# Kernel optimization log

Hardware: AMD Instinct MI355X
Metric: run time of the kernel (lower is better)

## Reference

```python
import jax, jax.numpy as jnp
import numpy as np

B, S, D, H, F = 2, 2048, 1024, 16, 4096
DK = D // H
EPS = 1e-6


def _ln(x, g, b):
    mu = jnp.mean(x, axis=-1, keepdims=True)
    var = jnp.mean(jnp.square(x - mu), axis=-1, keepdims=True)
    return (x - mu) * jax.lax.rsqrt(var + EPS) * g + b


def setup_inputs() -> dict:
    key = jax.random.key(0)
    ks = jax.random.split(key, 8)
    sc = 0.02
    return {
        "x": jax.random.normal(ks[0], (B, S, D), jnp.float32),
        "wq": jax.random.normal(ks[1], (D, D), jnp.float32) * sc,
        "bq": jnp.zeros((D,), jnp.float32),
        "wk": jax.random.normal(ks[2], (D, D), jnp.float32) * sc,
        "bk": jnp.zeros((D,), jnp.float32),
        "wv": jax.random.normal(ks[3], (D, D), jnp.float32) * sc,
        "bv": jnp.zeros((D,), jnp.float32),
        "wo": jax.random.normal(ks[4], (D, D), jnp.float32) * sc,
        "bo": jnp.zeros((D,), jnp.float32),
        "w1": jax.random.normal(ks[5], (D, F), jnp.float32) * sc,
        "b1": jnp.zeros((F,), jnp.float32),
        "w2": jax.random.normal(ks[6], (F, D), jnp.float32) * sc,
        "b2": jnp.zeros((D,), jnp.float32),
        "g1": jnp.ones((D,), jnp.float32),
        "be1": jnp.zeros((D,), jnp.float32),
        "g2": jnp.ones((D,), jnp.float32),
        "be2": jnp.zeros((D,), jnp.float32),
    }


def reference(x, wq, bq, wk, bk, wv, bv, wo, bo, w1, b1, w2, b2, g1, be1, g2, be2):
    # Multi-head self-attention (no masks, eval-mode dropout = identity)
    q = (x @ wq + bq).reshape(B, S, H, DK)
    k = (x @ wk + bk).reshape(B, S, H, DK)
    v = (x @ wv + bv).reshape(B, S, H, DK)
    scale = 1.0 / (DK ** 0.5)
    score = jnp.einsum('bihd,bjhd->bhij', q, k) * scale  # [B,H,S,S]
    p = jax.nn.softmax(score, axis=-1)
    attn = jnp.einsum('bhij,bjhd->bihd', p, v).reshape(B, S, D)
    attn = attn @ wo + bo
    # residual + LayerNorm 1
    h = _ln(x + attn, g1, be1)
    # FFN (relu) + residual + LayerNorm 2
    ff = jax.nn.relu(h @ w1 + b1) @ w2 + b2
    return _ln(h + ff, g2, be2)
```

## Files before the change

kernel.cpp:

```cpp
#include <hip/hip_runtime.h>
#include <hip/hip_bf16.h>
#include <cmath>

typedef __bf16 bf16_t;
typedef __bf16 bf16x4 __attribute__((ext_vector_type(4)));
typedef __bf16 bf16x8 __attribute__((ext_vector_type(8)));
typedef float  f32x4  __attribute__((ext_vector_type(4)));

__device__ __forceinline__ void gld_lds16(const bf16_t* g, bf16_t* l) {
    __builtin_amdgcn_global_load_lds(
        (const __attribute__((address_space(1))) void*)g,
        (__attribute__((address_space(3))) void*)l,
        16, 0, 0);
}

struct PrepArgs {
    const float* w[6]; bf16_t* wt[6];
    int K[6], N[6], start[6];
    const float* x; bf16_t* xb; int castStart;
    const float* bq; const float* bk; float* bqkv; int biasStart;
};

__global__ __launch_bounds__(256) void prep(PrepArgs pa) {
    __shared__ float tile[32][33];
    const int bid = blockIdx.x, t = threadIdx.x;
    if (bid < pa.castStart) {
        int mi = 0;
#pragma unroll
        for (int i = 1; i < 6; i++) if (bid >= pa.start[i]) mi = i;
        const int tt  = bid - pa.start[mi];
        const int nbx = pa.N[mi] >> 5;
        const int n0 = (tt % nbx) * 32, k0 = (tt / nbx) * 32;
        const float* in = pa.w[mi];
        bf16_t* out = pa.wt[mi];
        const int K = pa.K[mi], N = pa.N[mi];
        const int tx = t & 31, ty = t >> 5;
#pragma unroll
        for (int i = 0; i < 4; i++) {
            int kk = ty + i * 8;
            tile[kk][tx] = in[(size_t)(k0 + kk) * N + n0 + tx];
        }
        __syncthreads();
#pragma unroll
        for (int i = 0; i < 4; i++) {
            int nn = ty + i * 8;
            out[(size_t)(n0 + nn) * K + k0 + tx] = (bf16_t)tile[tx][nn];
        }
    } else if (bid < pa.biasStart) {
        int i = (bid - pa.castStart) * 256 + t;
        f32x4 v = ((const f32x4*)pa.x)[i];
        bf16x4 o;
        o[0] = (bf16_t)v[0]; o[1] = (bf16_t)v[1]; o[2] = (bf16_t)v[2]; o[3] = (bf16_t)v[3];
        ((bf16x4*)pa.xb)[i] = o;
    } else {
#pragma unroll
        for (int j = 0; j < 8; j++) {
            int idx = t * 8 + j;
            pa.bqkv[idx] = idx < 1024 ? pa.bq[idx] : pa.bk[idx - 1024];
        }
    }
}

template<int MT>
__global__ __launch_bounds__(256) void gemm_bt(
    const bf16_t* __restrict__ A, const bf16_t* __restrict__ Bt,
    const float* __restrict__ bias,
    float* __restrict__ Cf, bf16_t* __restrict__ Cb,
    int M, int N, int lda, int Kloc, int relu, int nbn, int bias_row,
    long bt_bstride, long c_bstride, int scale_cols, float scale) {
    constexpr int TM = MT * 32;
    __shared__ __attribute__((aligned(16))) bf16_t As[2][TM * 32];
    __shared__ __attribute__((aligned(16))) bf16_t Bs[2][128 * 32];
    const int tid  = threadIdx.x;
    const int lane = tid & 63;
    const int wave = tid >> 6;
    const int wm = wave & 1, wn = wave >> 1;
    const int kh = blockIdx.z;

    const int span  = 8 * nbn;
    const int group = blockIdx.x / span;
    const int rem   = blockIdx.x % span;
    const int bm    = group * 8 + (rem & 7);
    const int bn    = rem >> 3;

    const bf16_t* Bt_b = Bt + (size_t)blockIdx.y * bt_bstride;
    float*  Cf_b = Cf ? Cf + (size_t)blockIdx.y * c_bstride + (size_t)kh * M * N : nullptr;
    bf16_t* Cb_b = Cb ? Cb + (size_t)blockIdx.y * c_bstride : nullptr;
    const int koff = kh * Kloc;

    const int r4 = tid >> 2;
    const int kc = (tid & 3) * 8;
    const bf16_t* Ag = A    + (size_t)(bm * TM  + r4) * lda + koff + kc;
    const bf16_t* Bg = Bt_b + (size_t)(bn * 128 + r4) * lda + koff + kc;

    f32x4 acc[MT][4] = {};
    const int mrow = lane & 15;
    const int q8   = (lane >> 4) * 8;

    for (int k0 = 0; k0 < Kloc; k0 += 64) {
        __syncthreads();
#pragma unroll
        for (int hh = 0; hh < 2; hh++) {
#pragma unroll
            for (int i = 0; i < MT / 2; i++)
                gld_lds16(Ag + (size_t)(i * 64) * lda + k0 + hh * 32,
                          &As[hh][i * 64 * 32] + tid * 8);
            gld_lds16(Bg + k0 + hh * 32,                    &Bs[hh][0] + tid * 8);
            gld_lds16(Bg + (size_t)64 * lda + k0 + hh * 32, &Bs[hh][64 * 32] + tid * 8);
        }
        __syncthreads();

#pragma unroll
        for (int hh = 0; hh < 2; hh++) {
            bf16x8 af[MT], bfr[4];
#pragma unroll
            for (int mt = 0; mt < MT; mt++)
                af[mt] = *(const bf16x8*)(&As[hh][(wm * (MT * 16) + mt * 16 + mrow) * 32 + q8]);
#pragma unroll
            for (int nt = 0; nt < 4; nt++)
                bfr[nt] = *(const bf16x8*)(&Bs[hh][(wn * 64 + nt * 16 + mrow) * 32 + q8]);
#pragma unroll
            for (int mt = 0; mt < MT; mt++)
#pragma unroll
                for (int nt = 0; nt < 4; nt++)
                    acc[mt][nt] = __builtin_amdgcn_mfma_f32_16x16x32_bf16(
                        af[mt], bfr[nt], acc[mt][nt], 0, 0, 0);
        }
    }

    const int rq = (lane >> 4) * 4;
#pragma unroll
    for (int mt = 0; mt < MT; mt++) {
        int row0 = bm * TM + wm * (MT * 16) + mt * 16 + rq;
#pragma unroll
        for (int nt = 0; nt < 4; nt++) {
            int col = bn * 128 + wn * 64 + nt * 16 + mrow;
            float bvc = (bias && kh == 0 && !bias_row) ? bias[col] : 0.f;
            float sc = (col < scale_cols) ? scale : 1.f;
#pragma unroll
            for (int r = 0; r < 4; r++) {
                float bb = (bias && kh == 0 && bias_row) ? bias[row0 + r] : bvc;
                float v = acc[mt][nt][r] + bb;
                if (relu) v = fmaxf(v, 0.f);
                v *= sc;
                size_t idx = (size_t)(row0 + r) * N + col;
                if (Cf_b) Cf_b[idx] = v;
                if (Cb_b) Cb_b[idx] = (bf16_t)v;
            }
        }
    }
}

__global__ __launch_bounds__(256) void flash_attn_mfma(
    const bf16_t* __restrict__ QKb,
    const bf16_t* __restrict__ Vtg,
    bf16_t* __restrict__ Outb) {
    __shared__ __attribute__((aligned(16))) bf16_t QPs[64 * 72];
    __shared__ __attribute__((aligned(16))) bf16_t Ks[2][64 * 32];
    __shared__ __attribute__((aligned(16))) bf16_t Vs[2][64 * 32];
    const int t = threadIdx.x;
    const int lane = t & 63, wave = t >> 6;
    const int g = lane >> 4, cl = lane & 15;
    const int b = blockIdx.z, h = blockIdx.y, q0 = blockIdx.x * 64;
    const int RS = 2048;
    const bf16_t* Qg = QKb + (size_t)(b * 2048 + q0) * RS + h * 64;
    const bf16_t* Kg = QKb + (size_t)(b * 2048) * RS + 1024 + h * 64;
    const bf16_t* Vg = Vtg + ((size_t)b * 1024 + h * 64) * 2048;

    const int sr = t >> 2;
    const int sc = (t & 3) * 8;

    gld_lds16(Qg + (size_t)sr * RS + sc,      QPs + t * 8);
    gld_lds16(Qg + (size_t)sr * RS + 32 + sc, QPs + 2048 + t * 8);

    f32x4 Oacc[4] = {};
    f32x4 Lacc = {};
    bf16x8 ones;
#pragma unroll
    for (int j = 0; j < 8; j++) ones[j] = (bf16_t)1.0f;

    const int qrow_s = (wave * 16 + cl) * 32 + g * 8;
    const int prow_w = (wave * 16 + cl) * 72;

    __syncthreads();
    const bf16x8 bq0 = *(const bf16x8*)(QPs + qrow_s);
    const bf16x8 bq1 = *(const bf16x8*)(QPs + 2048 + qrow_s);

    for (int kt = 0; kt < 2048; kt += 64) {
        __syncthreads();
        gld_lds16(Kg + (size_t)(kt + sr) * RS + sc,      &Ks[0][0] + t * 8);
        gld_lds16(Kg + (size_t)(kt + sr) * RS + 32 + sc, &Ks[1][0] + t * 8);
        gld_lds16(Vg + (size_t)sr * 2048 + kt + sc,      &Vs[0][0] + t * 8);
        gld_lds16(Vg + (size_t)sr * 2048 + kt + 32 + sc, &Vs[1][0] + t * 8);
        __syncthreads();

        f32x4 Sacc[4] = {};
#pragma unroll
        for (int ks = 0; ks < 2; ks++) {
            const bf16x8 bq = ks ? bq1 : bq0;
#pragma unroll
            for (int mt = 0; mt < 4; mt++) {
                bf16x8 ak = *(const bf16x8*)(&Ks[ks][(mt * 16 + cl) * 32 + g * 8]);
                Sacc[mt] = __builtin_amdgcn_mfma_f32_16x16x32_bf16(ak, bq, Sacc[mt], 0, 0, 0);
            }
        }

#pragma unroll
        for (int mt = 0; mt < 4; mt++) {
            bf16x4 p4;
#pragma unroll
            for (int r = 0; r < 4; r++)
                p4[r] = (bf16_t)__builtin_amdgcn_exp2f(Sacc[mt][r]);
            *(bf16x4*)(QPs + prow_w + mt * 16 + g * 4) = p4;
        }

#pragma unroll
        for (int ks = 0; ks < 2; ks++) {
            bf16x8 ap = *(const bf16x8*)(QPs + prow_w + ks * 32 + g * 8);
            Lacc = __builtin_amdgcn_mfma_f32_16x16x32_bf16(ap, ones, Lacc, 0, 0, 0);
#pragma unroll
            for (int nt = 0; nt < 4; nt++) {
                bf16x8 bv = *(const bf16x8*)(&Vs[ks][(nt * 16 + cl) * 32 + g * 8]);
                Oacc[nt] = __builtin_amdgcn_mfma_f32_16x16x32_bf16(ap, bv, Oacc[nt], 0, 0, 0);
            }
        }
    }

#pragma unroll
    for (int r = 0; r < 4; r++) {
        float inv = 1.f / Lacc[r];
        int qrow = q0 + wave * 16 + g * 4 + r;
        size_t base = (size_t)(b * 2048 + qrow) * 1024 + h * 64;
#pragma unroll
        for (int nt = 0; nt < 4; nt++)
            Outb[base + nt * 16 + cl] = (bf16_t)(Oacc[nt][r] * inv);
    }
}

__global__ __launch_bounds__(256) void resid_ln3(const float* __restrict__ a,
                                                 const float* __restrict__ p0,
                                                 const float* __restrict__ p1,
                                                 const float* __restrict__ g,
                                                 const float* __restrict__ be,
                                                 float* __restrict__ outf,
                                                 bf16_t* __restrict__ outb) {
    const int row = blockIdx.x, t = threadIdx.x;
    const size_t base = (size_t)row * 1024;
    f32x4 v = ((const f32x4*)(a + base))[t] + ((const f32x4*)(p0 + base))[t];
    if (p1) v += ((const f32x4*)(p1 + base))[t];
    float sum = v[0] + v[1] + v[2] + v[3];
    float sq  = v[0] * v[0] + v[1] * v[1] + v[2] * v[2] + v[3] * v[3];
#pragma unroll
    for (int o = 1; o < 64; o <<= 1) {
        sum += __shfl_xor(sum, o);
        sq  += __shfl_xor(sq, o);
    }
    __shared__ float red[8];
    int wave = t >> 6, lane = t & 63;
    if (lane == 0) { red[wave] = sum; red[4 + wave] = sq; }
    __syncthreads();
    sum = red[0] + red[1] + red[2] + red[3];
    sq  = red[4] + red[5] + red[6] + red[7];
    float mu  = sum * (1.f / 1024.f);
    float var = sq * (1.f / 1024.f) - mu * mu;
    float rs  = rsqrtf(var + 1e-6f);
    f32x4 g4 = ((const f32x4*)g)[t];
    f32x4 b4 = ((const f32x4*)be)[t];
    f32x4 o = (v - mu) * rs * g4 + b4;
    ((f32x4*)(outf + base))[t] = o;
    if (outb) {
        bf16x4 ob;
        ob[0] = (bf16_t)o[0]; ob[1] = (bf16_t)o[1]; ob[2] = (bf16_t)o[2]; ob[3] = (bf16_t)o[3];
        ((bf16x4*)(outb + base))[t] = ob;
    }
}

extern "C" void kernel_launch(void* const* d_in, const int* in_sizes, int n_in,
                              void* d_out, int out_size, void* d_ws, size_t ws_size,
                              hipStream_t stream) {
    (void)in_sizes; (void)n_in; (void)out_size; (void)ws_size;
    const float* x   = (const float*)d_in[0];
    const float* wq  = (const float*)d_in[1];
    const float* bq  = (const float*)d_in[2];
    const float* wk  = (const float*)d_in[3];
    const float* bk  = (const float*)d_in[4];
    const float* wv  = (const float*)d_in[5];
    const float* bv  = (const float*)d_in[6];
    const float* wo  = (const float*)d_in[7];
    const float* bo  = (const float*)d_in[8];
    const float* w1  = (const float*)d_in[9];
    const float* b1  = (const float*)d_in[10];
    const float* w2  = (const float*)d_in[11];
    const float* b2  = (const float*)d_in[12];
    const float* g1  = (const float*)d_in[13];
    const float* be1 = (const float*)d_in[14];
    const float* g2  = (const float*)d_in[15];
    const float* be2 = (const float*)d_in[16];
    float* out = (float*)d_out;

    char* ws = (char*)d_ws;
    const size_t MB = 1ull << 20;
    bf16_t* xb    = (bf16_t*)(ws + 0);
    bf16_t* WtQKV = (bf16_t*)(ws + 8 * MB);
    bf16_t* WtO   = (bf16_t*)(ws + 14 * MB);
    bf16_t* Wt1   = (bf16_t*)(ws + 16 * MB);
    bf16_t* Wt2   = (bf16_t*)(ws + 24 * MB);
    float*  bqkv  = (float*)(ws + 32 * MB);
    bf16_t* QKb   = (bf16_t*)(ws + 33 * MB);
    bf16_t* Vt    = (bf16_t*)(ws + 49 * MB);
    bf16_t* ffb   = (bf16_t*)(ws + 33 * MB);
    float*  oa    = (float*)(ws + 65 * MB);
    float*  f2    = (float*)(ws + 65 * MB);
    float*  hbuf  = (float*)(ws + 97 * MB);
    bf16_t* hb    = (bf16_t*)(ws + 113 * MB);
    bf16_t* ab    = xb;
    const int MN = 4096 * 1024;
    const float Cs = 0.125f * 1.4426950408889634f;

    PrepArgs pa;
    pa.w[0] = wq; pa.w[1] = wk; pa.w[2] = wv; pa.w[3] = wo; pa.w[4] = w1; pa.w[5] = w2;
    pa.wt[0] = WtQKV; pa.wt[1] = WtQKV + 1024 * 1024; pa.wt[2] = WtQKV + 2048 * 1024;
    pa.wt[3] = WtO; pa.wt[4] = Wt1; pa.wt[5] = Wt2;
    int Ks[6] = {1024, 1024, 1024, 1024, 1024, 4096};
    int Ns[6] = {1024, 1024, 1024, 1024, 4096, 1024};
    int st[6] = {0, 1024, 2048, 3072, 4096, 8192};
    for (int i = 0; i < 6; i++) { pa.K[i] = Ks[i]; pa.N[i] = Ns[i]; pa.start[i] = st[i]; }
    pa.x = x; pa.xb = xb; pa.castStart = 12288;
    pa.bq = bq; pa.bk = bk; pa.bqkv = bqkv; pa.biasStart = 12288 + 4096;
    prep<<<12288 + 4096 + 1, 256, 0, stream>>>(pa);

    gemm_bt<4><<<512, 256, 0, stream>>>(xb, WtQKV, bqkv, nullptr, QKb,
                                        4096, 2048, 1024, 1024, 0, 16, 0, 0, 0,
                                        1024, Cs);
    gemm_bt<2><<<dim3(256, 2, 1), 256, 0, stream>>>(WtQKV + 2048 * 1024, xb, bv,
                                        nullptr, Vt, 1024, 2048, 1024, 1024, 0, 16, 1,
                                        (long)2048 * 1024, (long)1024 * 2048, 0, 1.f);
    flash_attn_mfma<<<dim3(32, 16, 2), 256, 0, stream>>>(QKb, Vt, ab);
    gemm_bt<4><<<dim3(256, 1, 2), 256, 0, stream>>>(ab, WtO, bo, oa, nullptr,
                                        4096, 1024, 1024, 512, 0, 8, 0, 0, 0, 0, 1.f);
    resid_ln3<<<4096, 256, 0, stream>>>(x, oa, oa + MN, g1, be1, hbuf, hb);
    gemm_bt<4><<<1024, 256, 0, stream>>>(hb, Wt1, b1, nullptr, ffb,
                                         4096, 4096, 1024, 1024, 1, 32, 0, 0, 0, 0, 1.f);
    gemm_bt<4><<<dim3(256, 1, 2), 256, 0, stream>>>(ffb, Wt2, b2, f2, nullptr,
                                        4096, 1024, 4096, 2048, 0, 8, 0, 0, 0, 0, 1.f);
    resid_ln3<<<4096, 256, 0, stream>>>(hbuf, f2, f2 + MN, g2, be2, out, nullptr);
}
```

Measured before the change: 415.2 us.

## Merge QK and V projection GEMMs into one launch; widen attention blocks to 128 queries

Folds the QK projection GEMM and the transposed V projection GEMM into a single dual-descriptor kernel, so one grid of 768 blocks covers both. The V GEMM now uses the MT=4 tile instead of MT=2. Flash attention blocks grow to 512 threads handling 128 queries, so each K/V tile staged into LDS is shared by eight waves instead of four. This halves K/V global traffic per query and removes a launch, at the cost of fewer attention blocks and more LDS and threads per block.

```diff
diff --git a/kernel.cpp b/kernel.cpp
--- a/kernel.cpp
+++ b/kernel.cpp
@@ -61,52 +61,53 @@
     }
 }
 
+struct GemmDesc {
+    const bf16_t* A; const bf16_t* Bt; const float* bias;
+    float* Cf; bf16_t* Cb;
+    int M, N, lda, Kloc, relu, nbn, bias_row;
+    long bt_bstride, c_bstride;
+    int scale_cols; float scale;
+};
+
 template<int MT>
-__global__ __launch_bounds__(256) void gemm_bt(
-    const bf16_t* __restrict__ A, const bf16_t* __restrict__ Bt,
-    const float* __restrict__ bias,
-    float* __restrict__ Cf, bf16_t* __restrict__ Cb,
-    int M, int N, int lda, int Kloc, int relu, int nbn, int bias_row,
-    long bt_bstride, long c_bstride, int scale_cols, float scale) {
+__device__ __forceinline__ void gemm_core(const GemmDesc& d, int bidx, int batch,
+                                          int kh, bf16_t* As, bf16_t* Bs) {
     constexpr int TM = MT * 32;
-    __shared__ __attribute__((aligned(16))) bf16_t As[2][TM * 32];
-    __shared__ __attribute__((aligned(16))) bf16_t Bs[2][128 * 32];
     const int tid  = threadIdx.x;
     const int lane = tid & 63;
     const int wave = tid >> 6;
     const int wm = wave & 1, wn = wave >> 1;
-    const int kh = blockIdx.z;
-
-    const int span  = 8 * nbn;
-    const int group = blockIdx.x / span;
-    const int rem   = blockIdx.x % span;
+
+    const int span  = 8 * d.nbn;
+    const int group = bidx / span;
+    const int rem   = bidx % span;
     const int bm    = group * 8 + (rem & 7);
     const int bn    = rem >> 3;
 
-    const bf16_t* Bt_b = Bt + (size_t)blockIdx.y * bt_bstride;
-    float*  Cf_b = Cf ? Cf + (size_t)blockIdx.y * c_bstride + (size_t)kh * M * N : nullptr;
-    bf16_t* Cb_b = Cb ? Cb + (size_t)blockIdx.y * c_bstride : nullptr;
-    const int koff = kh * Kloc;
+    const bf16_t* Bt_b = d.Bt + (size_t)batch * d.bt_bstride;
+    float*  Cf_b = d.Cf ? d.Cf + (size_t)batch * d.c_bstride + (size_t)kh * d.M * d.N : nullptr;
+    bf16_t* Cb_b = d.Cb ? d.Cb + (size_t)batch * d.c_bstride : nullptr;
+    const int koff = kh * d.Kloc;
 
     const int r4 = tid >> 2;
     const int kc = (tid & 3) * 8;
-    const bf16_t* Ag = A    + (size_t)(bm * TM  + r4) * lda + koff + kc;
-    const bf16_t* Bg = Bt_b + (size_t)(bn * 128 + r4) * lda + koff + kc;
+    const bf16_t* Ag = d.A  + (size_t)(bm * TM  + r4) * d.lda + koff + kc;
+    const bf16_t* Bg = Bt_b + (size_t)(bn * 128 + r4) * d.lda + koff + kc;
 
     f32x4 acc[MT][4] = {};
     const int mrow = lane & 15;
     const int q8   = (lane >> 4) * 8;
 
-    for (int k0 = 0; k0 < Kloc; k0 += 64) {
+    for (int k0 = 0; k0 < d.Kloc; k0 += 64) {
         __syncthreads();
 #pragma unroll
         for (int hh = 0; hh < 2; hh++) {
 #pragma unroll
             for (int i = 0; i < MT / 2; i++)
-                gld_lds16(Ag + (size_t)(i * 64) * lda + k0 + hh * 32,
-                          &As[hh][i * 64 * 32] + tid * 8);
-            gld_lds16(Bg + k0 + hh * 32,                    &Bs[hh][0] + tid * 8);
-            gld_lds16(Bg + (size_t)64 * lda + k0 + hh * 32, &Bs[hh][64 * 32] + tid * 8);
+                gld_lds16(Ag + (size_t)(i * 64) * d.lda + k0 + hh * 32,
+                          As + hh * (TM * 32) + i * 64 * 32 + tid * 8);
+            gld_lds16(Bg + k0 + hh * 32,                      Bs + hh * 4096 + tid * 8);
+            gld_lds16(Bg + (size_t)64 * d.lda + k0 + hh * 32, Bs + hh * 4096 + 64 * 32 + tid * 8);
         }
         __syncthreads();
 
@@ -115,10 +116,12 @@
             bf16x8 af[MT], bfr[4];
 #pragma unroll
             for (int mt = 0; mt < MT; mt++)
-                af[mt] = *(const bf16x8*)(&As[hh][(wm * (MT * 16) + mt * 16 + mrow) * 32 + q8]);
+                af[mt] = *(const bf16x8*)(As + hh * (TM * 32) +
+                                          (wm * (MT * 16) + mt * 16 + mrow) * 32 + q8);
 #pragma unroll
             for (int nt = 0; nt < 4; nt++)
-                bfr[nt] = *(const bf16x8*)(&Bs[hh][(wn * 64 + nt * 16 + mrow) * 32 + q8]);
+                bfr[nt] = *(const bf16x8*)(Bs + hh * 4096 +
+                                           (wn * 64 + nt * 16 + mrow) * 32 + q8);
 #pragma unroll
             for (int mt = 0; mt < MT; mt++)
 #pragma unroll
@@ -135,15 +138,15 @@
 #pragma unroll
         for (int nt = 0; nt < 4; nt++) {
             int col = bn * 128 + wn * 64 + nt * 16 + mrow;
-            float bvc = (bias && kh == 0 && !bias_row) ? bias[col] : 0.f;
-            float sc = (col < scale_cols) ? scale : 1.f;
+            float bvc = (d.bias && kh == 0 && !d.bias_row) ? d.bias[col] : 0.f;
+            float sc = (col < d.scale_cols) ? d.scale : 1.f;
 #pragma unroll
             for (int r = 0; r < 4; r++) {
-                float bb = (bias && kh == 0 && bias_row) ? bias[row0 + r] : bvc;
+                float bb = (d.bias && kh == 0 && d.bias_row) ? d.bias[row0 + r] : bvc;
                 float v = acc[mt][nt][r] + bb;
-                if (relu) v = fmaxf(v, 0.f);
+                if (d.relu) v = fmaxf(v, 0.f);
                 v *= sc;
-                size_t idx = (size_t)(row0 + r) * N + col;
+                size_t idx = (size_t)(row0 + r) * d.N + col;
                 if (Cf_b) Cf_b[idx] = v;
                 if (Cb_b) Cb_b[idx] = (bf16_t)v;
             }
@@ -151,27 +154,50 @@
     }
 }
 
-__global__ __launch_bounds__(256) void flash_attn_mfma(
+template<int MT>
+__global__ __launch_bounds__(256) void gemm_bt(GemmDesc d) {
+    __shared__ __attribute__((aligned(16))) bf16_t As[2 * MT * 32 * 32];
+    __shared__ __attribute__((aligned(16))) bf16_t Bs[2 * 128 * 32];
+    gemm_core<MT>(d, blockIdx.x, blockIdx.y, blockIdx.z, As, Bs);
+}
+
+__global__ __launch_bounds__(256) void gemm_dual(GemmDesc d0, int nblocks0,
+                                                 GemmDesc d1, int nblocks1) {
+    __shared__ __attribute__((aligned(16))) bf16_t As[2 * 128 * 32];
+    __shared__ __attribute__((aligned(16))) bf16_t Bs[2 * 128 * 32];
+    const int bid = blockIdx.x;
+    if (bid < nblocks0) {
+        gemm_core<4>(d0, bid, 0, 0, As, Bs);
+    } else {
+        int b2 = bid - nblocks0;
+        gemm_core<4>(d1, b2 % nblocks1, b2 / nblocks1, 0, As, Bs);
+    }
+}
+
+__global__ __launch_bounds__(512) void flash_attn_mfma(
     const bf16_t* __restrict__ QKb,
     const bf16_t* __restrict__ Vtg,
     bf16_t* __restrict__ Outb) {
-    __shared__ __attribute__((aligned(16))) bf16_t QPs[64 * 72];
+    __shared__ __attribute__((aligned(16))) bf16_t QPs[128 * 72];
     __shared__ __attribute__((aligned(16))) bf16_t Ks[2][64 * 32];
     __shared__ __attribute__((aligned(16))) bf16_t Vs[2][64 * 32];
     const int t = threadIdx.x;
     const int lane = t & 63, wave = t >> 6;
     const int g = lane >> 4, cl = lane & 15;
-    const int b = blockIdx.z, h = blockIdx.y, q0 = blockIdx.x * 64;
+    const int b = blockIdx.z, h = blockIdx.y, q0 = blockIdx.x * 128;
     const int RS = 2048;
     const bf16_t* Qg = QKb + (size_t)(b * 2048 + q0) * RS + h * 64;
     const bf16_t* Kg = QKb + (size_t)(b * 2048) * RS + 1024 + h * 64;
     const bf16_t* Vg = Vtg + ((size_t)b * 1024 + h * 64) * 2048;
 
-    const int sr = t >> 2;
-    const int sc = (t & 3) * 8;
-
-    gld_lds16(Qg + (size_t)sr * RS + sc,      QPs + t * 8);
-    gld_lds16(Qg + (size_t)sr * RS + 32 + sc, QPs + 2048 + t * 8);
+    {
+        int qr = t >> 2, qc = (t & 3) * 8;
+        gld_lds16(Qg + (size_t)qr * RS + qc,      QPs + t * 8);
+        gld_lds16(Qg + (size_t)qr * RS + 32 + qc, QPs + 4096 + t * 8);
+    }
+    const int kr = (t & 255) >> 2;
+    const int kc = (t & 3) * 8;
+    const int khf = (t >> 8) * 32;
 
     f32x4 Oacc[4] = {};
     f32x4 Lacc = {};
@@ -184,14 +210,12 @@
 
     __syncthreads();
     const bf16x8 bq0 = *(const bf16x8*)(QPs + qrow_s);
-    const bf16x8 bq1 = *(const bf16x8*)(QPs + 2048 + qrow_s);
+    const bf16x8 bq1 = *(const bf16x8*)(QPs + 4096 + qrow_s);
 
     for (int kt = 0; kt < 2048; kt += 64) {
         __syncthreads();
-        gld_lds16(Kg + (size_t)(kt + sr) * RS + sc,      &Ks[0][0] + t * 8);
-        gld_lds16(Kg + (size_t)(kt + sr) * RS + 32 + sc, &Ks[1][0] + t * 8);
-        gld_lds16(Vg + (size_t)sr * 2048 + kt + sc,      &Vs[0][0] + t * 8);
-        gld_lds16(Vg + (size_t)sr * 2048 + kt + 32 + sc, &Vs[1][0] + t * 8);
+        gld_lds16(Kg + (size_t)(kt + kr) * RS + khf + kc,  (bf16_t*)Ks + t * 8);
+        gld_lds16(Vg + (size_t)kr * 2048 + kt + khf + kc,  (bf16_t*)Vs + t * 8);
         __syncthreads();
 
         f32x4 Sacc[4] = {};
@@ -321,27 +345,36 @@
     pa.w[0] = wq; pa.w[1] = wk; pa.w[2] = wv; pa.w[3] = wo; pa.w[4] = w1; pa.w[5] = w2;
     pa.wt[0] = WtQKV; pa.wt[1] = WtQKV + 1024 * 1024; pa.wt[2] = WtQKV + 2048 * 1024;
     pa.wt[3] = WtO; pa.wt[4] = Wt1; pa.wt[5] = Wt2;
-    int Ks[6] = {1024, 1024, 1024, 1024, 1024, 4096};
-    int Ns[6] = {1024, 1024, 1024, 1024, 4096, 1024};
-    int st[6] = {0, 1024, 2048, 3072, 4096, 8192};
-    for (int i = 0; i < 6; i++) { pa.K[i] = Ks[i]; pa.N[i] = Ns[i]; pa.start[i] = st[i]; }
+    int Ksz[6] = {1024, 1024, 1024, 1024, 1024, 4096};
+    int Nsz[6] = {1024, 1024, 1024, 1024, 4096, 1024};
+    int st[6]  = {0, 1024, 2048, 3072, 4096, 8192};
+    for (int i = 0; i < 6; i++) { pa.K[i] = Ksz[i]; pa.N[i] = Nsz[i]; pa.start[i] = st[i]; }
     pa.x = x; pa.xb = xb; pa.castStart = 12288;
     pa.bq = bq; pa.bk = bk; pa.bqkv = bqkv; pa.biasStart = 12288 + 4096;
     prep<<<12288 + 4096 + 1, 256, 0, stream>>>(pa);
 
-    gemm_bt<4><<<512, 256, 0, stream>>>(xb, WtQKV, bqkv, nullptr, QKb,
-                                        4096, 2048, 1024, 1024, 0, 16, 0, 0, 0,
-                                        1024, Cs);
-    gemm_bt<2><<<dim3(256, 2, 1), 256, 0, stream>>>(WtQKV + 2048 * 1024, xb, bv,
-                                        nullptr, Vt, 1024, 2048, 1024, 1024, 0, 16, 1,
-                                        (long)2048 * 1024, (long)1024 * 2048, 0, 1.f);
-    flash_attn_mfma<<<dim3(32, 16, 2), 256, 0, stream>>>(QKb, Vt, ab);
-    gemm_bt<4><<<dim3(256, 1, 2), 256, 0, stream>>>(ab, WtO, bo, oa, nullptr,
-                                        4096, 1024, 1024, 512, 0, 8, 0, 0, 0, 0, 1.f);
+    GemmDesc dqk = { xb, WtQKV, bqkv, nullptr, QKb,
+                     4096, 2048, 1024, 1024, 0, 16, 0, 0, 0, 1024, Cs };
+    GemmDesc dv  = { WtQKV + 2048 * 1024, xb, bv, nullptr, Vt,
+                     1024, 2048, 1024, 1024, 0, 16, 1,
+                     (long)2048 * 1024, (long)1024 * 2048, 0, 1.f };
+    gemm_dual<<<768, 256, 0, stream>>>(dqk, 512, dv, 128);
+
+    flash_attn_mfma<<<dim3(16, 16, 2), 512, 0, stream>>>(QKb, Vt, ab);
+
+    GemmDesc dwo = { ab, WtO, bo, oa, nullptr,
+                     4096, 1024, 1024, 512, 0, 8, 0, 0, 0, 0, 1.f };
+    gemm_bt<4><<<dim3(256, 1, 2), 256, 0, stream>>>(dwo);
+
     resid_ln3<<<4096, 256, 0, stream>>>(x, oa, oa + MN, g1, be1, hbuf, hb);
-    gemm_bt<4><<<1024, 256, 0, stream>>>(hb, Wt1, b1, nullptr, ffb,
-                                         4096, 4096, 1024, 1024, 1, 32, 0, 0, 0, 0, 1.f);
-    gemm_bt<4><<<dim3(256, 1, 2), 256, 0, stream>>>(ffb, Wt2, b2, f2, nullptr,
-                                        4096, 1024, 4096, 2048, 0, 8, 0, 0, 0, 0, 1.f);
+
+    GemmDesc df1 = { hb, Wt1, b1, nullptr, ffb,
+                     4096, 4096, 1024, 1024, 1, 32, 0, 0, 0, 0, 1.f };
+    gemm_bt<4><<<1024, 256, 0, stream>>>(df1);
+
+    GemmDesc df2 = { ffb, Wt2, b2, f2, nullptr,
+                     4096, 1024, 4096, 2048, 0, 8, 0, 0, 0, 0, 1.f };
+    gemm_bt<4><<<dim3(256, 1, 2), 256, 0, stream>>>(df2);
+
     resid_ln3<<<4096, 256, 0, stream>>>(hbuf, f2, f2 + MN, g2, be2, out, nullptr);
 }
```

Result: no change. 418.7 us (+0.8%).
